# Performance work log

Measured on AMD Instinct MI355X. Metric: run time of the kernel, lower is better.

The kernel has to match this reference:

```python
import jax, jax.numpy as jnp
import numpy as np

HEADS = 8
BLOCK = 32

def setup_inputs() -> dict:
    key = jax.random.key(0)
    ks = jax.random.split(key, 4)
    b, n, d, f = 4, 4096, 1024, 128
    x = jax.random.normal(ks[0], (b, n, d), dtype=jnp.float32)
    w_qkv = jax.random.normal(ks[1], (3 * d, d), dtype=jnp.float32) * (d ** -0.5)
    w_out = jax.random.normal(ks[2], (d, d), dtype=jnp.float32) * (d ** -0.5)
    b_out = jnp.zeros((d,), dtype=jnp.float32)
    proj = jax.random.normal(ks[3], (HEADS, d // HEADS, f), dtype=jnp.float32) * ((d // HEADS) ** -0.5)
    return {"x": x, "w_qkv": w_qkv, "w_out": w_out, "b_out": b_out, "proj": proj}

def reference(x, w_qkv, w_out, b_out, proj):
    b, n, d = x.shape
    h = HEADS
    hd = d // h
    nb = n // BLOCK
    # QKV projection (torch Linear: x @ W.T)
    qkv = x @ w_qkv.T  # (b, n, 3d)
    q, k, v = jnp.split(qkv, 3, axis=-1)
    def to_blocks(t):
        # (b, n, d) -> (b, h, nb, BLOCK, hd)
        return t.reshape(b, n, h, hd).transpose(0, 2, 1, 3).reshape(b, h, nb, BLOCK, hd)
    q, k, v = to_blocks(q), to_blocks(k), to_blocks(v)
    # per-head feature map: elu(x @ proj) + 1
    qp = jax.nn.elu(jnp.einsum('bhcsd,hdf->bhcsf', q, proj)) + 1.0
    kp = jax.nn.elu(jnp.einsum('bhcsd,hdf->bhcsf', k, proj)) + 1.0
    # per-block kv state and normalizer
    kv = jnp.einsum('bhcsf,bhcsd->bhcfd', kp, v)          # (b,h,nb,f,hd)
    num = jnp.einsum('bhcsf,bhcfd->bhcsd', qp, kv)        # (b,h,nb,BLOCK,hd)
    ksum = kp.sum(axis=3)                                 # (b,h,nb,f)
    z = 1.0 / (jnp.einsum('bhcsf,bhcf->bhcs', qp, ksum) + 1e-8)
    out = num * z[..., None]
    # merge blocks and heads: (b,h,nb,BLOCK,hd) -> (b,n,d)
    out = out.reshape(b, h, n, hd).transpose(0, 2, 1, 3).reshape(b, n, d)
    # output projection (dropout inert in eval)
    return out @ w_out.T + b_out
```

## Files before the change

### kernel.cpp

```cpp
#include <hip/hip_runtime.h>
#include <hip/hip_bf16.h>
#include <stdint.h>
#include <stddef.h>

typedef __bf16 bf16_t;
typedef __bf16 bf16x8 __attribute__((ext_vector_type(8)));
typedef __bf16 bf16x4 __attribute__((ext_vector_type(4)));
typedef float  f32x4  __attribute__((ext_vector_type(4)));

static __device__ __forceinline__ f32x4 mfma16x16x32(bf16x8 a, bf16x8 b, f32x4 c) {
  return __builtin_amdgcn_mfma_f32_16x16x32_bf16(a, b, c, 0, 0, 0);
}

static __device__ __forceinline__ void gld_lds16(const void* g, void* l) {
  __builtin_amdgcn_global_load_lds(
      (const __attribute__((address_space(1))) unsigned int*)g,
      (__attribute__((address_space(3))) unsigned int*)l, 16, 0, 0);
}

#define BARW()   __builtin_amdgcn_s_barrier()
#define SCHED0() __builtin_amdgcn_sched_barrier(0)
#define LGKM0()  asm volatile("s_waitcnt lgkmcnt(0)" ::: "memory")
#define VMCNT(n) asm volatile("s_waitcnt vmcnt(" #n ")" ::: "memory")
#define PRIO(p)  __builtin_amdgcn_s_setprio(p)

__global__ __launch_bounds__(256) void cvt_bf16(const float* __restrict__ in,
                                                bf16_t* __restrict__ out, int n) {
  int stride = gridDim.x * blockDim.x;
  for (int i = blockIdx.x * blockDim.x + threadIdx.x; i * 4 < n; i += stride) {
    float4 v = *(const float4*)(in + (size_t)i * 4);
    bf16x4 o;
    o[0] = (bf16_t)v.x; o[1] = (bf16_t)v.y; o[2] = (bf16_t)v.z; o[3] = (bf16_t)v.w;
    *(bf16x4*)(out + (size_t)i * 4) = o;
  }
}

__global__ __launch_bounds__(256) void fuse_w(const float* __restrict__ wqkv,
                                              const float* __restrict__ proj,
                                              bf16_t* __restrict__ B1t2) {
  const int blk    = blockIdx.x;
  const int combo  = blk >> 4;
  const int kt     = blk & 15;
  const int qk     = combo >> 3;
  const int h      = combo & 7;
  const int klocal = threadIdx.x & 63;
  const int fg     = threadIdx.x >> 6;
  const int k      = kt * 64 + klocal;

  const float* wbase = wqkv + ((size_t)(qk * 1024 + h * 128)) * 1024 + k;
  const float* pbase = proj + (size_t)h * 16384 + fg * 32;

  float acc[32];
#pragma unroll
  for (int i = 0; i < 32; ++i) acc[i] = 0.f;

  for (int c = 0; c < 128; ++c) {
    float a = wbase[(size_t)c * 1024];
    const float4* p = (const float4*)(pbase + (size_t)c * 128);
#pragma unroll
    for (int i = 0; i < 8; ++i) {
      float4 pv = p[i];
      acc[i * 4 + 0] += a * pv.x;
      acc[i * 4 + 1] += a * pv.y;
      acc[i * 4 + 2] += a * pv.z;
      acc[i * 4 + 3] += a * pv.w;
    }
  }
  bf16_t* obase = B1t2 + ((size_t)(h * 256 + qk * 128 + fg * 32)) * 1024 + k;
#pragma unroll
  for (int i = 0; i < 32; ++i) obase[(size_t)i * 1024] = (bf16_t)acc[i];
}

#define GEMM_MAINLOOP_DECLS()                                                  \
  const int tid  = threadIdx.x;                                                \
  const int lane = tid & 63;                                                   \
  const int wid  = tid >> 6;                                                   \
  const int wm   = wid >> 2;                                                   \
  const int wn   = wid & 3;                                                    \
  const int lr   = lane & 15;                                                  \
  const int g0   = lane >> 4;                                                  \
  int srow[2], sgl[2];                                                         \
  _Pragma("unroll")                                                            \
  for (int l = 0; l < 2; ++l) {                                                \
    int idx = l * 512 + tid;                                                   \
    srow[l] = idx >> 3;                                                        \
    sgl[l]  = (idx & 7) ^ (srow[l] & 7);                                       \
  }

#define STAGE_T(arr, base, half, kt, K_)                                       \
  {                                                                            \
    const bf16_t* s_ = (base) + (size_t)((half) * 128) * (K_) + (kt) * 64;     \
    bf16_t* d_ = &(arr)[half][0];                                              \
    _Pragma("unroll")                                                          \
    for (int l_ = 0; l_ < 2; ++l_)                                             \
      gld_lds16(s_ + (size_t)srow[l_] * (K_) + sgl[l_] * 8,                    \
                d_ + (l_ * 512 + tid) * 8);                                    \
  }

#define RD_A(buf, qm)                                                          \
  _Pragma("unroll")                                                            \
  for (int t_ = 0; t_ < 4; ++t_) {                                             \
    int r_ = (qm) * 64 + t_ * 16 + lr;                                         \
    _Pragma("unroll")                                                          \
    for (int kh_ = 0; kh_ < 2; ++kh_) {                                        \
      int gl_ = (g0 + kh_ * 4) ^ (r_ & 7);                                     \
      a[t_][kh_] = *(const bf16x8*)(&sA[buf][wm][r_ * 64 + gl_ * 8]);          \
    }                                                                          \
  }
#define RD_B(buf, qn, breg)                                                    \
  _Pragma("unroll")                                                            \
  for (int u_ = 0; u_ < 2; ++u_) {                                             \
    int r_ = (wn & 1) * 64 + (qn) * 32 + u_ * 16 + lr;                         \
    _Pragma("unroll")                                                          \
    for (int kh_ = 0; kh_ < 2; ++kh_) {                                        \
      int gl_ = (g0 + kh_ * 4) ^ (r_ & 7);                                     \
      breg[u_][kh_] = *(const bf16x8*)(&sB[buf][wn >> 1][r_ * 64 + gl_ * 8]);  \
    }                                                                          \
  }
#define MMA(qm, qn, breg)                                                      \
  _Pragma("unroll")                                                            \
  for (int mi_ = 0; mi_ < 4; ++mi_)                                            \
    _Pragma("unroll")                                                          \
    for (int nj_ = 0; nj_ < 2; ++nj_)                                          \
      _Pragma("unroll")                                                        \
      for (int kh_ = 0; kh_ < 2; ++kh_)                                        \
        acc[(qm) * 4 + mi_][(qn) * 2 + nj_] =                                  \
            mfma16x16x32(a[mi_][kh_], breg[nj_][kh_],                          \
                         acc[(qm) * 4 + mi_][(qn) * 2 + nj_]);

#define GEMM_MAINLOOP_BODY(Abase, Bbase, K_, NT_)                              \
  f32x4 acc[8][4] = {};                                                        \
  bf16x8 a[4][2], b0[2][2], b1[2][2];                                          \
  STAGE_T(sA[0], Abase, 0, 0, K_); STAGE_T(sA[0], Abase, 1, 0, K_);            \
  STAGE_T(sB[0], Bbase, 0, 0, K_); STAGE_T(sB[0], Bbase, 1, 0, K_);            \
  STAGE_T(sA[1], Abase, 0, 1, K_); STAGE_T(sA[1], Abase, 1, 1, K_);            \
  STAGE_T(sB[1], Bbase, 0, 1, K_); STAGE_T(sB[1], Bbase, 1, 1, K_);            \
  VMCNT(8);                                                                    \
  BARW();                                                                      \
  _Pragma("unroll 2")                                                          \
  for (int j = 0; j < (NT_); ++j) {                                            \
    const int cur = j & 1;                                                     \
    const bool pf = (j + 2) < (NT_);                                           \
    RD_A(cur, 0);                                                              \
    RD_B(cur, 0, b0);                                                          \
    SCHED0(); BARW(); LGKM0(); SCHED0();                                       \
    PRIO(1); MMA(0, 0, b0); PRIO(0);                                           \
    SCHED0(); BARW();                                                          \
    RD_B(cur, 1, b1);                                                          \
    SCHED0(); BARW(); LGKM0(); SCHED0();                                       \
    PRIO(1); MMA(0, 1, b1); PRIO(0);                                           \
    SCHED0(); BARW();                                                          \
    RD_A(cur, 1);                                                              \
    if (pf) { STAGE_T(sB[cur], Bbase, 0, j + 2, K_); STAGE_T(sB[cur], Bbase, 1, j + 2, K_); } \
    SCHED0(); BARW(); LGKM0(); SCHED0();                                       \
    PRIO(1); MMA(1, 1, b1); PRIO(0);                                           \
    SCHED0(); BARW();                                                          \
    if (pf) { STAGE_T(sA[cur], Abase, 0, j + 2, K_); STAGE_T(sA[cur], Abase, 1, j + 2, K_); } \
    SCHED0(); BARW();                                                          \
    PRIO(1); MMA(1, 0, b0); PRIO(0);                                           \
    if (pf) { VMCNT(8); } else { VMCNT(0); }                                   \
    SCHED0(); BARW();                                                          \
  }

template <int EPI>
__global__ __launch_bounds__(512, 2) void gemm256(const bf16_t* __restrict__ A,
                                                  const bf16_t* __restrict__ Bt,
                                                  void* __restrict__ Cout,
                                                  const float* __restrict__ bias,
                                                  int N, int K, int NB) {
  __shared__ __align__(16) bf16_t sA[2][2][8192];
  __shared__ __align__(16) bf16_t sB[2][2][8192];
  GEMM_MAINLOOP_DECLS();

  const int nwg = gridDim.x;
  const int cpx = nwg >> 3;
  const int bid = blockIdx.x;
  const int swz = (bid & 7) * cpx + (bid >> 3);
  const int m0 = (swz / NB) * 256;
  const int n0 = (swz % NB) * 256;
  const int NT = K >> 6;

  const bf16_t* Abase = A  + (size_t)m0 * K;
  const bf16_t* Bbase = Bt + (size_t)n0 * K;

  GEMM_MAINLOOP_BODY(Abase, Bbase, K, NT);

#pragma unroll
  for (int i = 0; i < 8; ++i) {
#pragma unroll
    for (int jn = 0; jn < 4; ++jn) {
      const int n = n0 + wn * 64 + jn * 16 + lr;
#pragma unroll
      for (int r = 0; r < 4; ++r) {
        const int m = m0 + wm * 128 + i * 16 + g0 * 4 + r;
        float v = acc[i][jn][r];
        if constexpr (EPI == 2) {
          ((float*)Cout)[(size_t)m * N + n] = v + bias[n];
        } else {
          ((bf16_t*)Cout)[(size_t)m * N + n] = (bf16_t)v;
        }
      }
    }
  }
}

__global__ __launch_bounds__(512, 2) void gemm_fused(const bf16_t* __restrict__ A,
                                                     const bf16_t* __restrict__ Bt,
                                                     const bf16_t* __restrict__ VtG,
                                                     bf16_t* __restrict__ OUT1) {
  __shared__ __align__(16) bf16_t sA[2][2][8192];
  __shared__ __align__(16) bf16_t sB[2][2][8192];
  GEMM_MAINLOOP_DECLS();

  const int nwg = gridDim.x;
  const int cpx = nwg >> 3;
  const int bid = blockIdx.x;
  const int swz = (bid & 7) * cpx + (bid >> 3);
  const int m0 = (swz >> 3) * 256;
  const int h  = swz & 7;
  const int K  = 1024;
  const int NT = 16;

  const bf16_t* Abase = A  + (size_t)m0 * K;
  const bf16_t* Bbase = Bt + (size_t)(h * 256) * K;

  GEMM_MAINLOOP_BODY(Abase, Bbase, K, NT);

  char* sQb = (char*)(&sA[0][0][0]);
  char* sKb = (char*)(&sB[0][0][0]);

  {
    char* dbase = (wn < 2) ? sQb : sKb;
#pragma unroll
    for (int i = 0; i < 8; ++i)
#pragma unroll
      for (int jn = 0; jn < 4; ++jn)
#pragma unroll
        for (int r = 0; r < 4; ++r) {
          int row = wm * 128 + i * 16 + g0 * 4 + r;
          int col = (wn & 1) * 64 + jn * 16 + lr;
          float v = acc[i][jn][r];
          v = v > 0.f ? v + 1.f : __expf(v);
          int gq = col >> 3;
          int g  = (gq & 8) | ((gq ^ row) & 7);
          *(bf16_t*)(dbase + row * 256 + g * 16 + (col & 7) * 2) = (bf16_t)v;
        }
  }
  LGKM0();
  BARW();

  const int cb = wm * 4 + wn;
  const int rb = cb * 32;
  f32x4 sacc[2][2] = {};
#pragma unroll
  for (int kh = 0; kh < 4; ++kh) {
    bf16x8 aS[2], bS[2];
#pragma unroll
    for (int t = 0; t < 2; ++t) {
      int row = rb + t * 16 + lr;
      int gq = kh * 4 + g0;
      int g  = (gq & 8) | ((gq ^ row) & 7);
      aS[t] = *(const bf16x8*)(sQb + row * 256 + g * 16);
      bS[t] = *(const bf16x8*)(sKb + row * 256 + g * 16);
    }
#pragma unroll
    for (int mt = 0; mt < 2; ++mt)
#pragma unroll
      for (int nt = 0; nt < 2; ++nt)
        sacc[mt][nt] = mfma16x16x32(aS[mt], bS[nt], sacc[mt][nt]);
  }

  float zin[2][4];
#pragma unroll
  for (int mt = 0; mt < 2; ++mt)
#pragma unroll
    for (int r = 0; r < 4; ++r) {
      float s = sacc[mt][0][r] + sacc[mt][1][r];
      s += __shfl_xor(s, 1); s += __shfl_xor(s, 2);
      s += __shfl_xor(s, 4); s += __shfl_xor(s, 8);
      zin[mt][r] = 1.0f / (s + 1e-8f);
    }
  BARW();

  char* Pl = sQb;
#pragma unroll
  for (int mt = 0; mt < 2; ++mt)
#pragma unroll
    for (int nt = 0; nt < 2; ++nt)
#pragma unroll
      for (int r = 0; r < 4; ++r) {
        int i = mt * 16 + g0 * 4 + r;
        int jj = nt * 16 + lr;
        *(bf16_t*)(Pl + cb * 2560 + i * 80 + jj * 2) =
            (bf16_t)(sacc[mt][nt][r] * zin[mt][r]);
      }
  {
#pragma unroll
    for (int l = 0; l < 8; ++l) {
      int gd = l * 512 + tid;
      int row = gd >> 5, gcol = gd & 31;
      const bf16_t* src = VtG + (size_t)(h * 128 + row) * 16384 + m0 +
                          ((gcol ^ (row & 7)) * 8);
      gld_lds16(src, sKb + gd * 16);
    }
  }
  VMCNT(0);
  LGKM0();
  BARW();

  bf16x8 aP[2];
#pragma unroll
  for (int mt = 0; mt < 2; ++mt)
    aP[mt] = *(const bf16x8*)(Pl + cb * 2560 + (mt * 16 + lr) * 80 + g0 * 16);
#pragma unroll
  for (int dt = 0; dt < 8; ++dt) {
    int row = dt * 16 + lr;
    int gidx = cb * 4 + g0;
    int g = (gidx & 24) | ((gidx ^ row) & 7);
    bf16x8 bV = *(const bf16x8*)(sKb + row * 512 + g * 16);
#pragma unroll
    for (int mt = 0; mt < 2; ++mt) {
      f32x4 z = {};
      f32x4 o = mfma16x16x32(aP[mt], bV, z);
#pragma unroll
      for (int r = 0; r < 4; ++r) {
        int m = m0 + rb + mt * 16 + g0 * 4 + r;
        int d = h * 128 + dt * 16 + lr;
        OUT1[(size_t)m * 1024 + d] = (bf16_t)o[r];
      }
    }
  }
}

extern "C" void kernel_launch(void* const* d_in, const int* in_sizes, int n_in,
                              void* d_out, int out_size, void* d_ws, size_t ws_size,
                              hipStream_t stream) {
  const float* x     = (const float*)d_in[0];
  const float* w_qkv = (const float*)d_in[1];
  const float* w_out = (const float*)d_in[2];
  const float* b_out = (const float*)d_in[3];
  const float* proj  = (const float*)d_in[4];
  float* out = (float*)d_out;

  char* ws = (char*)d_ws;
  bf16_t* xbf  = (bf16_t*)(ws);
  bf16_t* B1t2 = (bf16_t*)(ws + 33554432);
  bf16_t* Wv   = (bf16_t*)(ws + 37748736);
  bf16_t* W3t  = (bf16_t*)(ws + 39845888);
  bf16_t* VtG  = (bf16_t*)(ws + 41943040);
  bf16_t* OUT1 = (bf16_t*)(ws + 75497472);

  (void)in_sizes; (void)n_in; (void)out_size; (void)ws_size;

  cvt_bf16<<<1024, 256, 0, stream>>>(x, xbf, 16777216);
  cvt_bf16<<<256, 256, 0, stream>>>(w_out, W3t, 1048576);
  cvt_bf16<<<256, 256, 0, stream>>>(w_qkv + (size_t)2048 * 1024, Wv, 1048576);
  fuse_w<<<256, 256, 0, stream>>>(w_qkv, proj, B1t2);
  gemm256<3><<<256, 512, 0, stream>>>(Wv, xbf, (void*)VtG, nullptr, 16384, 1024, 64);
  gemm_fused<<<512, 512, 0, stream>>>(xbf, B1t2, VtG, OUT1);
  gemm256<2><<<256, 512, 0, stream>>>(OUT1, W3t, (void*)out, b_out, 1024, 1024, 4);
}
```

Baseline: 238.9 us.

## Merge weight prep kernels, relax LDS waits, prefetch V during score MMA

Folds the two weight-conversion launches and the fused-weight kernel into a single prep kernel to cut launch overhead. In the GEMM main loop it adds partial lgkmcnt waits before barriers, so a wave waits only for its own earlier LDS traffic. In the fused attention kernel it loads all Q/K fragments into registers first, then issues the V tile global-to-LDS loads before the score MFMAs, overlapping the V fetch with compute and dropping one barrier. This raises register pressure, and the partial-wait counts must match the issued instruction counts to stay correct.

```diff
diff --git a/kernel.cpp b/kernel.cpp
--- a/kernel.cpp
+++ b/kernel.cpp
@@ -21,6 +21,7 @@
 #define BARW()   __builtin_amdgcn_s_barrier()
 #define SCHED0() __builtin_amdgcn_sched_barrier(0)
 #define LGKM0()  asm volatile("s_waitcnt lgkmcnt(0)" ::: "memory")
+#define LGKMN(n) asm volatile("s_waitcnt lgkmcnt(" #n ")" ::: "memory")
 #define VMCNT(n) asm volatile("s_waitcnt vmcnt(" #n ")" ::: "memory")
 #define PRIO(p)  __builtin_amdgcn_s_setprio(p)
 
@@ -35,16 +36,33 @@
   }
 }
 
-__global__ __launch_bounds__(256) void fuse_w(const float* __restrict__ wqkv,
-                                              const float* __restrict__ proj,
-                                              bf16_t* __restrict__ B1t2) {
-  const int blk    = blockIdx.x;
-  const int combo  = blk >> 4;
-  const int kt     = blk & 15;
+__global__ __launch_bounds__(256) void prep(const float* __restrict__ wqkv,
+                                            const float* __restrict__ proj,
+                                            const float* __restrict__ wout,
+                                            bf16_t* __restrict__ B1t2,
+                                            bf16_t* __restrict__ Wv,
+                                            bf16_t* __restrict__ W3t) {
+  const int b = blockIdx.x;
+  const int tid = threadIdx.x;
+  if (b >= 256) {
+    const float* src = (b < 512) ? wout : (wqkv + (size_t)2048 * 1024);
+    bf16_t* dst = (b < 512) ? W3t : Wv;
+    size_t off = ((size_t)((b & 255)) * 4096) + tid * 16;
+#pragma unroll
+    for (int it = 0; it < 4; ++it) {
+      float4 v = *(const float4*)(src + off + it * 4);
+      bf16x4 o;
+      o[0] = (bf16_t)v.x; o[1] = (bf16_t)v.y; o[2] = (bf16_t)v.z; o[3] = (bf16_t)v.w;
+      *(bf16x4*)(dst + off + it * 4) = o;
+    }
+    return;
+  }
+  const int combo  = b >> 4;
+  const int kt     = b & 15;
   const int qk     = combo >> 3;
   const int h      = combo & 7;
-  const int klocal = threadIdx.x & 63;
-  const int fg     = threadIdx.x >> 6;
+  const int klocal = tid & 63;
+  const int fg     = tid >> 6;
   const int k      = kt * 64 + klocal;
 
   const float* wbase = wqkv + ((size_t)(qk * 1024 + h * 128)) * 1024 + k;
@@ -143,7 +161,7 @@
     const bool pf = (j + 2) < (NT_);                                           \
     RD_A(cur, 0);                                                              \
     RD_B(cur, 0, b0);                                                          \
-    SCHED0(); BARW(); LGKM0(); SCHED0();                                       \
+    SCHED0(); LGKMN(8); BARW(); LGKM0(); SCHED0();                             \
     PRIO(1); MMA(0, 0, b0); PRIO(0);                                           \
     SCHED0(); BARW();                                                          \
     RD_B(cur, 1, b1);                                                          \
@@ -152,7 +170,7 @@
     SCHED0(); BARW();                                                          \
     RD_A(cur, 1);                                                              \
     if (pf) { STAGE_T(sB[cur], Bbase, 0, j + 2, K_); STAGE_T(sB[cur], Bbase, 1, j + 2, K_); } \
-    SCHED0(); BARW(); LGKM0(); SCHED0();                                       \
+    SCHED0(); LGKMN(4); BARW(); LGKM0(); SCHED0();                             \
     PRIO(1); MMA(1, 1, b1); PRIO(0);                                           \
     SCHED0(); BARW();                                                          \
     if (pf) { STAGE_T(sA[cur], Abase, 0, j + 2, K_); STAGE_T(sA[cur], Abase, 1, j + 2, K_); } \
@@ -251,24 +269,40 @@
 
   const int cb = wm * 4 + wn;
   const int rb = cb * 32;
-  f32x4 sacc[2][2] = {};
+  bf16x8 aS[4][2], bS[4][2];
 #pragma unroll
   for (int kh = 0; kh < 4; ++kh) {
-    bf16x8 aS[2], bS[2];
 #pragma unroll
     for (int t = 0; t < 2; ++t) {
       int row = rb + t * 16 + lr;
       int gq = kh * 4 + g0;
       int g  = (gq & 8) | ((gq ^ row) & 7);
-      aS[t] = *(const bf16x8*)(sQb + row * 256 + g * 16);
-      bS[t] = *(const bf16x8*)(sKb + row * 256 + g * 16);
-    }
+      aS[kh][t] = *(const bf16x8*)(sQb + row * 256 + g * 16);
+      bS[kh][t] = *(const bf16x8*)(sKb + row * 256 + g * 16);
+    }
+  }
+  SCHED0(); LGKM0(); BARW();
+
+  {
+#pragma unroll
+    for (int l = 0; l < 8; ++l) {
+      int gd = l * 512 + tid;
+      int row = gd >> 5, gcol = gd & 31;
+      const bf16_t* src = VtG + (size_t)(h * 128 + row) * 16384 + m0 +
+                          ((gcol ^ (row & 7)) * 8);
+      gld_lds16(src, sKb + gd * 16);
+    }
+  }
+  SCHED0();
+
+  f32x4 sacc[2][2] = {};
+#pragma unroll
+  for (int kh = 0; kh < 4; ++kh)
 #pragma unroll
     for (int mt = 0; mt < 2; ++mt)
 #pragma unroll
       for (int nt = 0; nt < 2; ++nt)
-        sacc[mt][nt] = mfma16x16x32(aS[mt], bS[nt], sacc[mt][nt]);
-  }
+        sacc[mt][nt] = mfma16x16x32(aS[kh][mt], bS[kh][nt], sacc[mt][nt]);
 
   float zin[2][4];
 #pragma unroll
@@ -280,7 +314,6 @@
       s += __shfl_xor(s, 4); s += __shfl_xor(s, 8);
       zin[mt][r] = 1.0f / (s + 1e-8f);
     }
-  BARW();
 
   char* Pl = sQb;
 #pragma unroll
@@ -294,18 +327,8 @@
         *(bf16_t*)(Pl + cb * 2560 + i * 80 + jj * 2) =
             (bf16_t)(sacc[mt][nt][r] * zin[mt][r]);
       }
-  {
-#pragma unroll
-    for (int l = 0; l < 8; ++l) {
-      int gd = l * 512 + tid;
-      int row = gd >> 5, gcol = gd & 31;
-      const bf16_t* src = VtG + (size_t)(h * 128 + row) * 16384 + m0 +
-                          ((gcol ^ (row & 7)) * 8);
-      gld_lds16(src, sKb + gd * 16);
-    }
-  }
+  LGKM0();
   VMCNT(0);
-  LGKM0();
   BARW();
 
   bf16x8 aP[2];
@@ -352,10 +375,8 @@
 
   (void)in_sizes; (void)n_in; (void)out_size; (void)ws_size;
 
+  prep<<<768, 256, 0, stream>>>(w_qkv, proj, w_out, B1t2, Wv, W3t);
   cvt_bf16<<<1024, 256, 0, stream>>>(x, xbf, 16777216);
-  cvt_bf16<<<256, 256, 0, stream>>>(w_out, W3t, 1048576);
-  cvt_bf16<<<256, 256, 0, stream>>>(w_qkv + (size_t)2048 * 1024, Wv, 1048576);
-  fuse_w<<<256, 256, 0, stream>>>(w_qkv, proj, B1t2);
   gemm256<3><<<256, 512, 0, stream>>>(Wv, xbf, (void*)VtG, nullptr, 16384, 1024, 64);
   gemm_fused<<<512, 512, 0, stream>>>(xbf, B1t2, VtG, OUT1);
   gemm256<2><<<256, 512, 0, stream>>>(OUT1, W3t, (void*)out, b_out, 1024, 1024, 4);
```

Result: no change. 235.0 us (-1.6%).
